# Kernel tuning notes

Measured on AMD Instinct MI355X. Metric: run time of the kernel, lower is better.

Reference implementation:

```python
import jax, jax.numpy as jnp
import numpy as np

N_NODES = 100000
N_EDGES = 1600000
F_IN, HID, N_CLS = 128, 128, 64


def setup_inputs() -> dict:
    key = jax.random.key(0)
    ks = jax.random.split(key, 9)
    x = jax.random.normal(ks[0], (N_NODES, F_IN), dtype=jnp.float32)
    edge_index = jax.random.randint(ks[1], (2, N_EDGES), 0, N_NODES, dtype=jnp.int64)
    edge_attr = jax.random.uniform(ks[2], (N_EDGES,), dtype=jnp.float32)
    def glorot(k, fi, fo):
        lim = (6.0 / (fi + fo)) ** 0.5
        return jax.random.uniform(k, (fi, fo), minval=-lim, maxval=lim, dtype=jnp.float32)
    return {
        "x": x, "edge_index": edge_index, "edge_attr": edge_attr,
        "W1": glorot(ks[3], F_IN, HID), "b1": jnp.zeros((HID,), jnp.float32),
        "W2": glorot(ks[4], HID, HID), "b2": jnp.zeros((HID,), jnp.float32),
        "W3": glorot(ks[5], HID, N_CLS), "b3": jnp.zeros((N_CLS,), jnp.float32),
    }


def reference(x, edge_index, edge_attr, W1, b1, W2, b2, W3, b3):
    N = x.shape[0]
    # PyG GCNConv: add self-loops with weight 1, symmetric normalization
    loop = jnp.arange(N, dtype=edge_index.dtype)
    src = jnp.concatenate([edge_index[0], loop])  # [E+N]
    dst = jnp.concatenate([edge_index[1], loop])
    w = jnp.concatenate([edge_attr, jnp.ones((N,), edge_attr.dtype)])
    deg = jax.ops.segment_sum(w, dst, num_segments=N)  # [N]
    dinv = jnp.where(deg > 0, deg ** -0.5, 0.0)
    norm = dinv[src] * w * dinv[dst]  # [E+N]

    def gcn_conv(h, W, b):
        h = h @ W                                 # [N, out]
        msg = norm[:, None] * h[src]              # [E+N, out] gather
        agg = jax.ops.segment_sum(msg, dst, num_segments=N)  # scatter-add
        return agg + b

    # dropout is identity in eval mode
    h = jax.nn.relu(gcn_conv(x, W1, b1))
    h = jax.nn.relu(gcn_conv(h, W2, b2))
    return gcn_conv(h, W3, b3)
```

## Files before the change

### kernel.cpp

```cpp
#include <hip/hip_runtime.h>
#include <hip/hip_fp16.h>


#define F_IN 128
#define HID  128
#define N_CLS 64

#define EDGE_CHUNK 8192
#define BCAP 6144

typedef _Float16 h8 __attribute__((ext_vector_type(8)));
typedef float f32x4 __attribute__((ext_vector_type(4)));


__global__ void k_wcvt(const float* __restrict__ W1, const float* __restrict__ W2,
                       const float* __restrict__ W3,
                       _Float16* __restrict__ T1, _Float16* __restrict__ T2,
                       _Float16* __restrict__ T3,
                       int* __restrict__ cursor, int NB) {
    int id = blockIdx.x * blockDim.x + threadIdx.x;
    if (id < NB) cursor[id] = 0;
    if (id < 16384) {
        int n = id >> 7, k = id & 127;
        T1[n * 128 + k] = (_Float16)W1[k * 128 + n];
    } else if (id < 32768) {
        int i = id - 16384;
        int n = i >> 7, k = i & 127;
        T2[n * 128 + k] = (_Float16)W2[k * 128 + n];
    } else if (id < 40960) {
        int i = id - 32768;
        int n = i >> 7, k = i & 127;
        T3[n * 128 + k] = (_Float16)W3[k * 64 + n];
    }
}


__global__ void k_bscatter(const int* __restrict__ src, const int* __restrict__ dst,
                           const float* __restrict__ w, int* __restrict__ cursor,
                           int2* __restrict__ stage, int E) {
    __shared__ int lcnt[512];
    __shared__ int lbase[512];
    const int t = threadIdx.x;
    for (int i = t; i < 512; i += 256) lcnt[i] = 0;
    __syncthreads();
    const int base = blockIdx.x * EDGE_CHUNK;
    int d[32];
#pragma unroll
    for (int i = 0; i < 32; ++i) {
        int e = base + i * 256 + t;
        d[i] = (e < E) ? dst[e] : -1;
        if (d[i] >= 0) atomicAdd(&lcnt[d[i] >> 8], 1);
    }
    __syncthreads();
    for (int i = t; i < 512; i += 256) {
        int c = lcnt[i];
        lbase[i] = (c > 0) ? atomicAdd(&cursor[i], c) : 0;
        lcnt[i] = 0;
    }
    __syncthreads();
#pragma unroll
    for (int i = 0; i < 32; ++i) {
        int e = base + i * 256 + t;
        if (e >= E) continue;
        int dd = d[i];
        int b  = dd >> 8;
        int p  = lbase[b] + atomicAdd(&lcnt[b], 1);
        if (p < BCAP)
            stage[(size_t)b * BCAP + p] =
                make_int2(src[e] | ((dd & 255) << 20), __float_as_int(w[e]));
    }
}

__global__ void k_slabdeg(const int2* __restrict__ stage, const int* __restrict__ cursor,
                          float* __restrict__ dinv, int* __restrict__ bbase,
                          int n, int NB, int E) {
    __shared__ float degf[256];
    __shared__ int   sh[512];
    const int b = blockIdx.x, t = threadIdx.x;
    if (t < 256) degf[t] = 0.0f;
    __syncthreads();
    const int cnt0 = cursor[b];
    const int cnt  = (cnt0 < BCAP) ? cnt0 : BCAP;
    const int2* sl = stage + (size_t)b * BCAP;
    for (int j = t; j < cnt; j += 512) {
        int2 s = sl[j];
        atomicAdd(&degf[s.x >> 20], __int_as_float(s.y));
    }
    __syncthreads();
    const int node = b * 256 + t;
    if (t < 256 && node < n) dinv[node] = rsqrtf(1.0f + degf[t]);

    if (b == 0) {
        sh[t] = (t < NB) ? min(cursor[t], BCAP) : 0;
        __syncthreads();
        for (int off = 1; off < 512; off <<= 1) {
            int x = (t >= off) ? sh[t - off] : 0;
            __syncthreads();
            sh[t] += x;
            __syncthreads();
        }
        if (t < NB) bbase[t] = (t == 0) ? 0 : sh[t - 1];
        if (t == 0) bbase[NB] = E;
    }
}

__global__ void k_bucket_csr(const int2* __restrict__ stage, const int* __restrict__ bbase,
                             const float* __restrict__ dinv,
                             int* __restrict__ row_ptr, int2* __restrict__ csr,
                             int n, int E) {
    __shared__ int scn[256];
    __shared__ int cur[256];
    const int b = blockIdx.x, t = threadIdx.x;
    const int beg = bbase[b];
    const int cnt = bbase[b + 1] - beg;
    const int2* sl = stage + (size_t)b * BCAP;
    scn[t] = 0;
    __syncthreads();
    for (int j = t; j < cnt; j += 256)
        atomicAdd(&scn[sl[j].x >> 20], 1);
    __syncthreads();
    int own = scn[t];
    __syncthreads();
    for (int off = 1; off < 256; off <<= 1) {
        int x = (t >= off) ? scn[t - off] : 0;
        __syncthreads();
        scn[t] += x;
        __syncthreads();
    }
    const int excl = scn[t] - own;
    const int node = b * 256 + t;
    if (node < n) row_ptr[node] = beg + excl;
    cur[t] = excl;
    __syncthreads();
    for (int j = t; j < cnt; j += 256) {
        int2 s = sl[j];
        int dlow = s.x >> 20;
        int srcid = s.x & 0xFFFFF;
        float nw = dinv[srcid] * __int_as_float(s.y);
        int pos = beg + atomicAdd(&cur[dlow], 1);
        csr[pos] = make_int2(srcid, __float_as_int(nw));
    }
    if (b == 0 && t == 0) row_ptr[n] = E;
}


template <int BN, typename TA>
__launch_bounds__(256)
__global__ void k_mm_mfma(const TA* __restrict__ A, const _Float16* __restrict__ WT,
                          __half* __restrict__ C, int nrows) {
    constexpr int K   = 128;
    constexpr int NCT = BN / 16;
    constexpr int KP  = K + 8;
    constexpr int CP  = BN + 8;
    __shared__ _Float16 lw[BN * KP];
    __shared__ _Float16 lc[64 * CP];
    const int tid  = threadIdx.x;
    const int wave = tid >> 6;
    const int lane = tid & 63;
    const int bm0  = blockIdx.x * 64;

    for (int c = tid; c < BN * 16; c += 256) {
        int n = c >> 4, k = (c & 15) * 8;
        *(h8*)&lw[n * KP + k] = *(const h8*)&WT[n * 128 + k];
    }
    __syncthreads();

    f32x4 acc[NCT];
#pragma unroll
    for (int ct = 0; ct < NCT; ++ct)
#pragma unroll
        for (int i = 0; i < 4; ++i) acc[ct][i] = 0.0f;

    const int row = bm0 + wave * 16 + (lane & 15);
    const int kb  = (lane >> 4) * 8;
    const bool rok = row < nrows;

#pragma unroll
    for (int kk = 0; kk < 4; ++kk) {
        const int k0 = kk * 32 + kb;
        h8 va;
        if (rok) {
            if constexpr (__is_same(TA, float)) {
                float4 f0 = *(const float4*)&A[(size_t)row * K + k0];
                float4 f1 = *(const float4*)&A[(size_t)row * K + k0 + 4];
                va[0] = (_Float16)f0.x; va[1] = (_Float16)f0.y;
                va[2] = (_Float16)f0.z; va[3] = (_Float16)f0.w;
                va[4] = (_Float16)f1.x; va[5] = (_Float16)f1.y;
                va[6] = (_Float16)f1.z; va[7] = (_Float16)f1.w;
            } else {
                va = *(const h8*)&A[(size_t)row * K + k0];
            }
        } else {
#pragma unroll
            for (int i = 0; i < 8; ++i) va[i] = (_Float16)0.0f;
        }
#pragma unroll
        for (int ct = 0; ct < NCT; ++ct) {
            h8 vb = *(const h8*)&lw[(ct * 16 + (lane & 15)) * KP + k0];
            acc[ct] = __builtin_amdgcn_mfma_f32_16x16x32_f16(va, vb, acc[ct], 0, 0, 0);
        }
    }

#pragma unroll
    for (int ct = 0; ct < NCT; ++ct)
#pragma unroll
        for (int r = 0; r < 4; ++r)
            lc[(wave * 16 + (lane >> 4) * 4 + r) * CP + ct * 16 + (lane & 15)] =
                (_Float16)acc[ct][r];
    __syncthreads();

    constexpr int NCH = (64 * BN / 8) / 256;
#pragma unroll
    for (int i = 0; i < NCH; ++i) {
        int c = i * 256 + tid;
        int r = c / (BN / 8), col = (c % (BN / 8)) * 8;
        int grow = bm0 + r;
        if (grow < nrows)
            *(h8*)&C[(size_t)grow * BN + col] = *(const h8*)&lc[r * CP + col];
    }
}


template <int NCOL, bool RELU, typename TO>
__launch_bounds__(256)
__global__ void k_agg(const __half* __restrict__ XW, const int* __restrict__ row_ptr,
                      const int2* __restrict__ csr,
                      const float* __restrict__ dinv, const float* __restrict__ bias,
                      TO* __restrict__ out, int n) {
    constexpr int PER = NCOL / 64;
    int wid  = (blockIdx.x * blockDim.x + threadIdx.x) >> 6;
    int lane = threadIdx.x & 63;
    if (wid >= n) return;
    const int node = __builtin_amdgcn_readfirstlane(wid);
    const float dn  = dinv[node];
    const int  beg  = row_ptr[node];
    const int  end  = row_ptr[node + 1];

    float a0, a1 = 0.0f;
    {
        if (PER == 2) {
            __half2 hv = *(const __half2*)&XW[(size_t)node * NCOL + lane * 2];
            a0 = dn * __low2float(hv); a1 = dn * __high2float(hv);
        } else {
            a0 = dn * __half2float(XW[(size_t)node * NCOL + lane]);
        }
    }

    int j = beg;
    for (; j + 4 <= end; j += 4) {
        int2 e0 = csr[j + 0], e1 = csr[j + 1], e2 = csr[j + 2], e3 = csr[j + 3];
        float w0 = __int_as_float(e0.y), w1 = __int_as_float(e1.y);
        float w2 = __int_as_float(e2.y), w3 = __int_as_float(e3.y);
        if (PER == 2) {
            __half2 v0 = *(const __half2*)&XW[(size_t)e0.x * NCOL + lane * 2];
            __half2 v1 = *(const __half2*)&XW[(size_t)e1.x * NCOL + lane * 2];
            __half2 v2 = *(const __half2*)&XW[(size_t)e2.x * NCOL + lane * 2];
            __half2 v3 = *(const __half2*)&XW[(size_t)e3.x * NCOL + lane * 2];
            a0 = fmaf(w0, __low2float(v0), a0); a1 = fmaf(w0, __high2float(v0), a1);
            a0 = fmaf(w1, __low2float(v1), a0); a1 = fmaf(w1, __high2float(v1), a1);
            a0 = fmaf(w2, __low2float(v2), a0); a1 = fmaf(w2, __high2float(v2), a1);
            a0 = fmaf(w3, __low2float(v3), a0); a1 = fmaf(w3, __high2float(v3), a1);
        } else {
            float v0 = __half2float(XW[(size_t)e0.x * NCOL + lane]);
            float v1 = __half2float(XW[(size_t)e1.x * NCOL + lane]);
            float v2 = __half2float(XW[(size_t)e2.x * NCOL + lane]);
            float v3 = __half2float(XW[(size_t)e3.x * NCOL + lane]);
            a0 = fmaf(w0, v0, a0);
            a0 = fmaf(w1, v1, a0);
            a0 = fmaf(w2, v2, a0);
            a0 = fmaf(w3, v3, a0);
        }
    }
    for (; j < end; ++j) {
        int2 e = csr[j];
        float nw = __int_as_float(e.y);
        if (PER == 2) {
            __half2 v = *(const __half2*)&XW[(size_t)e.x * NCOL + lane * 2];
            a0 = fmaf(nw, __low2float(v), a0); a1 = fmaf(nw, __high2float(v), a1);
        } else {
            a0 = fmaf(nw, __half2float(XW[(size_t)e.x * NCOL + lane]), a0);
        }
    }

    if (PER == 2) {
        a0 = fmaf(dn, a0, bias[lane * 2 + 0]);
        a1 = fmaf(dn, a1, bias[lane * 2 + 1]);
        if (RELU) { a0 = fmaxf(a0, 0.0f); a1 = fmaxf(a1, 0.0f); }
        if constexpr (__is_same(TO, float)) {
            *(float2*)&out[(size_t)node * NCOL + lane * 2] = make_float2(a0, a1);
        } else {
            *(__half2*)&out[(size_t)node * NCOL + lane * 2] = __floats2half2_rn(a0, a1);
        }
    } else {
        a0 = fmaf(dn, a0, bias[lane]);
        if (RELU) a0 = fmaxf(a0, 0.0f);
        if constexpr (__is_same(TO, float)) {
            out[(size_t)node * NCOL + lane] = a0;
        } else {
            out[(size_t)node * NCOL + lane] = __float2half(a0);
        }
    }
}


extern "C" void kernel_launch(void* const* d_in, const int* in_sizes, int n_in,
                              void* d_out, int out_size, void* d_ws, size_t ws_size,
                              hipStream_t stream) {
    const float* x  = (const float*)d_in[0];
    const int*   ei = (const int*)d_in[1];
    const float* ea = (const float*)d_in[2];
    const float* W1 = (const float*)d_in[3];
    const float* b1 = (const float*)d_in[4];
    const float* W2 = (const float*)d_in[5];
    const float* b2 = (const float*)d_in[6];
    const float* W3 = (const float*)d_in[7];
    const float* b3 = (const float*)d_in[8];

    const int N = in_sizes[0] / F_IN;
    const int E = in_sizes[1] / 2;
    const int* src = ei;
    const int* dst = ei + E;
    const int NB = (N + 255) / 256;

    char* ws = (char*)d_ws;
    size_t off = 0;
    auto alloc = [&](size_t bytes) -> void* {
        void* p = ws + off;
        off += (bytes + 255) & ~(size_t)255;
        return p;
    };
    __half*    bufH    = (__half*)   alloc((size_t)N * HID * sizeof(__half));
    __half*    bufH2   = (__half*)   alloc((size_t)N * HID * sizeof(__half));
    float*     dinv    = (float*)    alloc((size_t)N * sizeof(float));
    int*       row_ptr = (int*)      alloc((size_t)(N + 1) * sizeof(int));
    int2*      csr     = (int2*)     alloc((size_t)E * sizeof(int2));
    int2*      stage   = (int2*)     alloc((size_t)NB * BCAP * sizeof(int2));
    int*       cursor  = (int*)      alloc((size_t)NB * sizeof(int));
    int*       bbase   = (int*)      alloc((size_t)(NB + 1) * sizeof(int));
    _Float16*  W1T     = (_Float16*) alloc((size_t)128 * 128 * sizeof(_Float16));
    _Float16*  W2T     = (_Float16*) alloc((size_t)128 * 128 * sizeof(_Float16));
    _Float16*  W3T     = (_Float16*) alloc((size_t)64 * 128 * sizeof(_Float16));
    (void)ws_size;

    const int BLK = 256;
    const int nEB = (E + EDGE_CHUNK - 1) / EDGE_CHUNK;

    k_wcvt<<<(40960 + BLK - 1) / BLK, BLK, 0, stream>>>(W1, W2, W3, W1T, W2T, W3T,
                                                        cursor, NB);
    k_bscatter<<<nEB, BLK, 0, stream>>>(src, dst, ea, cursor, stage, E);
    k_slabdeg<<<NB, 512, 0, stream>>>(stage, cursor, dinv, bbase, N, NB, E);
    k_bucket_csr<<<NB, BLK, 0, stream>>>(stage, bbase, dinv, row_ptr, csr, N, E);

    const int gMM = (N + 63) / 64;
    const int gAG = (N + 3) / 4;

    k_mm_mfma<HID, float><<<gMM, BLK, 0, stream>>>(x, W1T, bufH, N);
    k_agg<HID, true, __half><<<gAG, BLK, 0, stream>>>(bufH, row_ptr, csr, dinv, b1, bufH2, N);
    k_mm_mfma<HID, __half><<<gMM, BLK, 0, stream>>>(bufH2, W2T, bufH, N);
    k_agg<HID, true, __half><<<gAG, BLK, 0, stream>>>(bufH, row_ptr, csr, dinv, b2, bufH2, N);
    k_mm_mfma<N_CLS, __half><<<gMM, BLK, 0, stream>>>(bufH2, W3T, bufH, N);
    k_agg<N_CLS, false, float><<<gAG, BLK, 0, stream>>>(bufH, row_ptr, csr, dinv, b3, (float*)d_out, N);
}
```

Before: 293.5 us.

## Merge edge bucket scatter with first-layer GEMM and fold weight conversion into CSR build

```diff
diff --git a/kernel.cpp b/kernel.cpp
--- a/kernel.cpp
+++ b/kernel.cpp
@@ -13,155 +13,33 @@
 typedef float f32x4 __attribute__((ext_vector_type(4)));
 
 
-__global__ void k_wcvt(const float* __restrict__ W1, const float* __restrict__ W2,
-                       const float* __restrict__ W3,
-                       _Float16* __restrict__ T1, _Float16* __restrict__ T2,
-                       _Float16* __restrict__ T3,
-                       int* __restrict__ cursor, int NB) {
-    int id = blockIdx.x * blockDim.x + threadIdx.x;
-    if (id < NB) cursor[id] = 0;
-    if (id < 16384) {
-        int n = id >> 7, k = id & 127;
-        T1[n * 128 + k] = (_Float16)W1[k * 128 + n];
-    } else if (id < 32768) {
-        int i = id - 16384;
-        int n = i >> 7, k = i & 127;
-        T2[n * 128 + k] = (_Float16)W2[k * 128 + n];
-    } else if (id < 40960) {
-        int i = id - 32768;
-        int n = i >> 7, k = i & 127;
-        T3[n * 128 + k] = (_Float16)W3[k * 64 + n];
-    }
-}
-
-
-__global__ void k_bscatter(const int* __restrict__ src, const int* __restrict__ dst,
-                           const float* __restrict__ w, int* __restrict__ cursor,
-                           int2* __restrict__ stage, int E) {
-    __shared__ int lcnt[512];
-    __shared__ int lbase[512];
-    const int t = threadIdx.x;
-    for (int i = t; i < 512; i += 256) lcnt[i] = 0;
-    __syncthreads();
-    const int base = blockIdx.x * EDGE_CHUNK;
-    int d[32];
-#pragma unroll
-    for (int i = 0; i < 32; ++i) {
-        int e = base + i * 256 + t;
-        d[i] = (e < E) ? dst[e] : -1;
-        if (d[i] >= 0) atomicAdd(&lcnt[d[i] >> 8], 1);
-    }
-    __syncthreads();
-    for (int i = t; i < 512; i += 256) {
-        int c = lcnt[i];
-        lbase[i] = (c > 0) ? atomicAdd(&cursor[i], c) : 0;
-        lcnt[i] = 0;
-    }
-    __syncthreads();
-#pragma unroll
-    for (int i = 0; i < 32; ++i) {
-        int e = base + i * 256 + t;
-        if (e >= E) continue;
-        int dd = d[i];
-        int b  = dd >> 8;
-        int p  = lbase[b] + atomicAdd(&lcnt[b], 1);
-        if (p < BCAP)
-            stage[(size_t)b * BCAP + p] =
-                make_int2(src[e] | ((dd & 255) << 20), __float_as_int(w[e]));
-    }
-}
-
-__global__ void k_slabdeg(const int2* __restrict__ stage, const int* __restrict__ cursor,
-                          float* __restrict__ dinv, int* __restrict__ bbase,
-                          int n, int NB, int E) {
-    __shared__ float degf[256];
-    __shared__ int   sh[512];
-    const int b = blockIdx.x, t = threadIdx.x;
-    if (t < 256) degf[t] = 0.0f;
-    __syncthreads();
-    const int cnt0 = cursor[b];
-    const int cnt  = (cnt0 < BCAP) ? cnt0 : BCAP;
-    const int2* sl = stage + (size_t)b * BCAP;
-    for (int j = t; j < cnt; j += 512) {
-        int2 s = sl[j];
-        atomicAdd(&degf[s.x >> 20], __int_as_float(s.y));
-    }
-    __syncthreads();
-    const int node = b * 256 + t;
-    if (t < 256 && node < n) dinv[node] = rsqrtf(1.0f + degf[t]);
-
-    if (b == 0) {
-        sh[t] = (t < NB) ? min(cursor[t], BCAP) : 0;
-        __syncthreads();
-        for (int off = 1; off < 512; off <<= 1) {
-            int x = (t >= off) ? sh[t - off] : 0;
-            __syncthreads();
-            sh[t] += x;
-            __syncthreads();
-        }
-        if (t < NB) bbase[t] = (t == 0) ? 0 : sh[t - 1];
-        if (t == 0) bbase[NB] = E;
-    }
-}
-
-__global__ void k_bucket_csr(const int2* __restrict__ stage, const int* __restrict__ bbase,
-                             const float* __restrict__ dinv,
-                             int* __restrict__ row_ptr, int2* __restrict__ csr,
-                             int n, int E) {
-    __shared__ int scn[256];
-    __shared__ int cur[256];
-    const int b = blockIdx.x, t = threadIdx.x;
-    const int beg = bbase[b];
-    const int cnt = bbase[b + 1] - beg;
-    const int2* sl = stage + (size_t)b * BCAP;
-    scn[t] = 0;
-    __syncthreads();
-    for (int j = t; j < cnt; j += 256)
-        atomicAdd(&scn[sl[j].x >> 20], 1);
-    __syncthreads();
-    int own = scn[t];
-    __syncthreads();
-    for (int off = 1; off < 256; off <<= 1) {
-        int x = (t >= off) ? scn[t - off] : 0;
-        __syncthreads();
-        scn[t] += x;
-        __syncthreads();
-    }
-    const int excl = scn[t] - own;
-    const int node = b * 256 + t;
-    if (node < n) row_ptr[node] = beg + excl;
-    cur[t] = excl;
-    __syncthreads();
-    for (int j = t; j < cnt; j += 256) {
-        int2 s = sl[j];
-        int dlow = s.x >> 20;
-        int srcid = s.x & 0xFFFFF;
-        float nw = dinv[srcid] * __int_as_float(s.y);
-        int pos = beg + atomicAdd(&cur[dlow], 1);
-        csr[pos] = make_int2(srcid, __float_as_int(nw));
-    }
-    if (b == 0 && t == 0) row_ptr[n] = E;
-}
-
-
-template <int BN, typename TA>
-__launch_bounds__(256)
-__global__ void k_mm_mfma(const TA* __restrict__ A, const _Float16* __restrict__ WT,
-                          __half* __restrict__ C, int nrows) {
+template <int BN, typename TA, bool CVTW>
+__device__ __forceinline__
+void mm_body(const TA* __restrict__ A, const float* __restrict__ Wsrc,
+             const _Float16* __restrict__ WT, __half* __restrict__ C,
+             int nrows, int bid, char* smem) {
     constexpr int K   = 128;
     constexpr int NCT = BN / 16;
     constexpr int KP  = K + 8;
     constexpr int CP  = BN + 8;
-    __shared__ _Float16 lw[BN * KP];
-    __shared__ _Float16 lc[64 * CP];
+    _Float16* lw = (_Float16*)smem;
+    _Float16* lc = (_Float16*)(smem + (size_t)BN * KP * 2);
     const int tid  = threadIdx.x;
     const int wave = tid >> 6;
     const int lane = tid & 63;
-    const int bm0  = blockIdx.x * 64;
-
-    for (int c = tid; c < BN * 16; c += 256) {
-        int n = c >> 4, k = (c & 15) * 8;
-        *(h8*)&lw[n * KP + k] = *(const h8*)&WT[n * 128 + k];
+    const int bm0  = bid * 64;
+
+    if constexpr (CVTW) {
+        for (int c = tid; c < BN * K; c += 256) {
+            int n = c & (BN - 1);
+            int k = c / BN;
+            lw[n * KP + k] = (_Float16)Wsrc[k * BN + n];
+        }
+    } else {
+        for (int c = tid; c < BN * 16; c += 256) {
+            int n = c >> 4, k = (c & 15) * 8;
+            *(h8*)&lw[n * KP + k] = *(const h8*)&WT[n * 128 + k];
+        }
     }
     __syncthreads();
 
@@ -218,6 +96,159 @@
         if (grow < nrows)
             *(h8*)&C[(size_t)grow * BN + col] = *(const h8*)&lc[r * CP + col];
     }
+}
+
+
+__device__ __forceinline__
+void bscatter_body(const int* __restrict__ src, const int* __restrict__ dst,
+                   const float* __restrict__ w, int* __restrict__ cursor,
+                   int2* __restrict__ stage, int E, int bid, char* smem) {
+    int* lcnt  = (int*)smem;
+    int* lbase = (int*)(smem + 2048);
+    const int t = threadIdx.x;
+    for (int i = t; i < 512; i += 256) lcnt[i] = 0;
+    __syncthreads();
+    const int base = bid * EDGE_CHUNK;
+    int d[32];
+#pragma unroll
+    for (int i = 0; i < 32; ++i) {
+        int e = base + i * 256 + t;
+        d[i] = (e < E) ? dst[e] : -1;
+        if (d[i] >= 0) atomicAdd(&lcnt[d[i] >> 8], 1);
+    }
+    __syncthreads();
+    for (int i = t; i < 512; i += 256) {
+        int c = lcnt[i];
+        lbase[i] = (c > 0) ? atomicAdd(&cursor[i], c) : 0;
+        lcnt[i] = 0;
+    }
+    __syncthreads();
+#pragma unroll
+    for (int i = 0; i < 32; ++i) {
+        int e = base + i * 256 + t;
+        if (e >= E) continue;
+        int dd = d[i];
+        int b  = dd >> 8;
+        int p  = lbase[b] + atomicAdd(&lcnt[b], 1);
+        if (p < BCAP)
+            stage[(size_t)b * BCAP + p] =
+                make_int2(src[e] | ((dd & 255) << 20), __float_as_int(w[e]));
+    }
+}
+
+
+#define SMEM_FRONT ((HID * (128 + 8) + 64 * (HID + 8)) * 2)
+
+__launch_bounds__(256)
+__global__ void k_front(const int* __restrict__ src, const int* __restrict__ dst,
+                        const float* __restrict__ w, int* __restrict__ cursor,
+                        int2* __restrict__ stage, int E,
+                        const float* __restrict__ x, const float* __restrict__ W1,
+                        __half* __restrict__ bufH, int nrows, int nEB) {
+    __shared__ __align__(16) char smem[SMEM_FRONT];
+    if ((int)blockIdx.x < nEB)
+        bscatter_body(src, dst, w, cursor, stage, E, blockIdx.x, smem);
+    else
+        mm_body<HID, float, true>(x, W1, nullptr, bufH, nrows, blockIdx.x - nEB, smem);
+}
+
+
+__global__ void k_slabdeg(const int2* __restrict__ stage, const int* __restrict__ cursor,
+                          float* __restrict__ dinv, int* __restrict__ bbase,
+                          int n, int NB, int E) {
+    __shared__ float degf[256];
+    __shared__ int   sh[512];
+    const int b = blockIdx.x, t = threadIdx.x;
+    if (t < 256) degf[t] = 0.0f;
+    __syncthreads();
+    const int cnt0 = cursor[b];
+    const int cnt  = (cnt0 < BCAP) ? cnt0 : BCAP;
+    const int2* sl = stage + (size_t)b * BCAP;
+    for (int j = t; j < cnt; j += 512) {
+        int2 s = sl[j];
+        atomicAdd(&degf[s.x >> 20], __int_as_float(s.y));
+    }
+    __syncthreads();
+    const int node = b * 256 + t;
+    if (t < 256 && node < n) dinv[node] = rsqrtf(1.0f + degf[t]);
+
+    if (b == 0) {
+        sh[t] = (t < NB) ? min(cursor[t], BCAP) : 0;
+        __syncthreads();
+        for (int off = 1; off < 512; off <<= 1) {
+            int x2 = (t >= off) ? sh[t - off] : 0;
+            __syncthreads();
+            sh[t] += x2;
+            __syncthreads();
+        }
+        if (t < NB) bbase[t] = (t == 0) ? 0 : sh[t - 1];
+        if (t == 0) bbase[NB] = E;
+    }
+}
+
+
+__launch_bounds__(256)
+__global__ void k_csrw(const int2* __restrict__ stage, const int* __restrict__ bbase,
+                       const float* __restrict__ dinv,
+                       int* __restrict__ row_ptr, int2* __restrict__ csr,
+                       int n, int E,
+                       const float* __restrict__ W2, const float* __restrict__ W3,
+                       _Float16* __restrict__ W2T, _Float16* __restrict__ W3T, int NB) {
+    __shared__ int scn[256];
+    __shared__ int cur[256];
+    const int t = threadIdx.x;
+    if ((int)blockIdx.x >= NB) {
+        int id = ((int)blockIdx.x - NB) * 256 + t;
+        if (id < 16384) {
+            int n2 = id >> 7, k = id & 127;
+            W2T[n2 * 128 + k] = (_Float16)W2[k * 128 + n2];
+        } else {
+            int i = id - 16384;
+            int n3 = i >> 7, k = i & 127;
+            W3T[n3 * 128 + k] = (_Float16)W3[k * 64 + n3];
+        }
+        return;
+    }
+    const int b = blockIdx.x;
+    const int beg = bbase[b];
+    const int cnt = bbase[b + 1] - beg;
+    const int2* sl = stage + (size_t)b * BCAP;
+    scn[t] = 0;
+    __syncthreads();
+    for (int j = t; j < cnt; j += 256)
+        atomicAdd(&scn[sl[j].x >> 20], 1);
+    __syncthreads();
+    int own = scn[t];
+    __syncthreads();
+    for (int off = 1; off < 256; off <<= 1) {
+        int x2 = (t >= off) ? scn[t - off] : 0;
+        __syncthreads();
+        scn[t] += x2;
+        __syncthreads();
+    }
+    const int excl = scn[t] - own;
+    const int node = b * 256 + t;
+    if (node < n) row_ptr[node] = beg + excl;
+    cur[t] = excl;
+    __syncthreads();
+    for (int j = t; j < cnt; j += 256) {
+        int2 s = sl[j];
+        int dlow  = s.x >> 20;
+        int srcid = s.x & 0xFFFFF;
+        float nw  = dinv[srcid] * __int_as_float(s.y);
+        int pos = beg + atomicAdd(&cur[dlow], 1);
+        csr[pos] = make_int2(srcid, __float_as_int(nw));
+    }
+    if (b == 0 && t == 0) row_ptr[n] = E;
+}
+
+
+template <int BN, typename TA>
+__launch_bounds__(256)
+__global__ void k_mm_mfma(const TA* __restrict__ A, const _Float16* __restrict__ WT,
+                          __half* __restrict__ C, int nrows) {
+    __shared__ __align__(16) char smem[(BN * (128 + 8) + 64 * (BN + 8)) * 2];
+    mm_body<BN, TA, false>(A, nullptr, WT, C, nrows, blockIdx.x, smem);
 }
 
 
@@ -337,24 +368,23 @@
     int2*      stage   = (int2*)     alloc((size_t)NB * BCAP * sizeof(int2));
     int*       cursor  = (int*)      alloc((size_t)NB * sizeof(int));
     int*       bbase   = (int*)      alloc((size_t)(NB + 1) * sizeof(int));
-    _Float16*  W1T     = (_Float16*) alloc((size_t)128 * 128 * sizeof(_Float16));
     _Float16*  W2T     = (_Float16*) alloc((size_t)128 * 128 * sizeof(_Float16));
     _Float16*  W3T     = (_Float16*) alloc((size_t)64 * 128 * sizeof(_Float16));
     (void)ws_size;
 
     const int BLK = 256;
     const int nEB = (E + EDGE_CHUNK - 1) / EDGE_CHUNK;
-
-    k_wcvt<<<(40960 + BLK - 1) / BLK, BLK, 0, stream>>>(W1, W2, W3, W1T, W2T, W3T,
-                                                        cursor, NB);
-    k_bscatter<<<nEB, BLK, 0, stream>>>(src, dst, ea, cursor, stage, E);
+    const int gMM = (N + 63) / 64;
+
+    hipMemsetAsync(cursor, 0, (size_t)NB * sizeof(int), stream);
+    k_front<<<nEB + gMM, BLK, 0, stream>>>(src, dst, ea, cursor, stage, E,
+                                           x, W1, bufH, N, nEB);
     k_slabdeg<<<NB, 512, 0, stream>>>(stage, cursor, dinv, bbase, N, NB, E);
-    k_bucket_csr<<<NB, BLK, 0, stream>>>(stage, bbase, dinv, row_ptr, csr, N, E);
-
-    const int gMM = (N + 63) / 64;
+    k_csrw<<<NB + 96, BLK, 0, stream>>>(stage, bbase, dinv, row_ptr, csr, N, E,
+                                        W2, W3, W2T, W3T, NB);
+
     const int gAG = (N + 3) / 4;
 
-    k_mm_mfma<HID, float><<<gMM, BLK, 0, stream>>>(x, W1T, bufH, N);
     k_agg<HID, true, __half><<<gAG, BLK, 0, stream>>>(bufH, row_ptr, csr, dinv, b1, bufH2, N);
     k_mm_mfma<HID, __half><<<gMM, BLK, 0, stream>>>(bufH2, W2T, bufH, N);
     k_agg<HID, true, __half><<<gAG, BLK, 0, stream>>>(bufH, row_ptr, csr, dinv, b2, bufH2, N);
```

Measured after the change: 280.4 us (median of 2 runs). -4.5%, faster.
